# Performance work log

Measured on AMD Instinct MI355X. Metric: run time of the kernel, lower is better.

## Reference

```python
import jax, jax.numpy as jnp
import numpy as np

B, S, E, H = 8, 1024, 1024, 16
D = E // H  # per-head dim = 64
STD = 0.05  # nn.init.normal_ std used in the torch module


def setup_inputs() -> dict:
    key = jax.random.key(0)
    ks = jax.random.split(key, 9)
    inputs = jax.random.normal(ks[0], (B, S, E), dtype=jnp.float32)
    mlp_params_Q = jax.random.normal(ks[1], (B, E), dtype=jnp.float32)
    mlp_params_K = jax.random.normal(ks[2], (B, E), dtype=jnp.float32)
    W_Query = jax.random.normal(ks[3], (E, E), dtype=jnp.float32) * STD
    W_Key = jax.random.normal(ks[4], (E, E), dtype=jnp.float32) * STD
    W_Value = jax.random.normal(ks[5], (E, E), dtype=jnp.float32) * STD
    W_Out = jax.random.normal(ks[6], (E, E), dtype=jnp.float32) * STD  # nn.Linear weight [out, in]
    ln_gamma = jax.random.normal(ks[7], (E,), dtype=jnp.float32) * STD
    ln_beta = jax.random.normal(ks[8], (E,), dtype=jnp.float32) * STD
    return {"inputs": inputs, "mlp_params_Q": mlp_params_Q, "mlp_params_K": mlp_params_K,
            "W_Query": W_Query, "W_Key": W_Key, "W_Value": W_Value, "W_Out": W_Out,
            "ln_gamma": ln_gamma, "ln_beta": ln_beta}


def reference(inputs, mlp_params_Q, mlp_params_K, W_Query, W_Key, W_Value, W_Out, ln_gamma, ln_beta):
    # QKV projections: [B,S,E] @ [E,E]
    q = jnp.einsum('bse,ef->bsf', inputs, W_Query)
    k = jnp.einsum('bse,ef->bsf', inputs, W_Key)
    v = jnp.einsum('bse,ef->bsf', inputs, W_Value)
    # meta gate modulation (flag='gate', mode='QK'): per-batch channel gates, *2
    q = q * mlp_params_Q[:, None, :] * 2.0
    k = k * mlp_params_K[:, None, :] * 2.0
    # split heads: channels [h*D:(h+1)*D] -> head h (matches torch.split/stack)
    qh = q.reshape(B, S, H, D)
    kh = k.reshape(B, S, H, D)
    vh = v.reshape(B, S, H, D)
    # attention scores [B,H,S,S], scaled by sqrt(D)
    scores = jnp.einsum('bihd,bjhd->bhij', qh, kh) / jnp.sqrt(jnp.asarray(D, q.dtype))
    attn = jax.nn.softmax(scores, axis=-1)  # attn_dropout is identity at eval
    out = jnp.einsum('bhij,bjhd->bihd', attn, vh).reshape(B, S, E)  # concat heads
    # output projection (nn.Linear, no bias): x @ W.T; dropout identity at eval
    res = jnp.einsum('bse,fe->bsf', out, W_Out)
    # residual + LayerNorm(eps=1e-6)
    res = res + inputs
    mean = jnp.mean(res, axis=-1, keepdims=True)
    var = jnp.mean(jnp.square(res - mean), axis=-1, keepdims=True)
    res = (res - mean) * jax.lax.rsqrt(var + 1e-6) * ln_gamma + ln_beta
    return res
```

## Files before the change

### kernel.cpp

```cpp
#include <hip/hip_runtime.h>
#include <stdint.h>

#define Bn 8
#define Sn 1024
#define En 1024
#define Hn 16
#define Dn 64
#define Mn (Bn*Sn)

typedef unsigned short u16;
typedef _Float16 f16;
typedef _Float16 f16x8 __attribute__((ext_vector_type(8)));
typedef __fp16   h16x2 __attribute__((ext_vector_type(2)));
typedef float    f32x4 __attribute__((ext_vector_type(4)));

static __device__ __forceinline__ u16 f2h(float x){
  f16 h = (f16)x;
  union { f16 h; u16 u; } c; c.h = h; return c.u;
}
static __device__ __forceinline__ f32x4 mfma16(f16x8 a, f16x8 b, f32x4 c){
  return __builtin_amdgcn_mfma_f32_16x16x32_f16(a, b, c, 0, 0, 0);
}
static __device__ __forceinline__ void gl_lds16(const u16* g, u16* l){
  __builtin_amdgcn_global_load_lds((__attribute__((address_space(1))) void*)g,
                                   (__attribute__((address_space(3))) void*)l, 16, 0, 0);
}

__global__ __launch_bounds__(256) void k_cvt_x(const float* __restrict__ x,
                                               u16* __restrict__ o){
  int i = blockIdx.x*256 + threadIdx.x;
  float4 v = ((const float4*)x)[i];
  ushort4 h; h.x = f2h(v.x); h.y = f2h(v.y); h.z = f2h(v.z); h.w = f2h(v.w);
  ((ushort4*)o)[i] = h;
}

__global__ __launch_bounds__(256) void k_prep_w(const float* __restrict__ Wq,
    const float* __restrict__ Wk, const float* __restrict__ Wv,
    u16* __restrict__ wq, u16* __restrict__ wk, u16* __restrict__ wv){
  __shared__ float t[32][33];
  int tx = threadIdx.x & 31, ty = threadIdx.x >> 5;
  int bx = blockIdx.x & 31, by = blockIdx.x >> 5;
  const float* W = (blockIdx.y == 0) ? Wq : (blockIdx.y == 1) ? Wk : Wv;
  u16* D = (blockIdx.y == 0) ? wq : (blockIdx.y == 1) ? wk : wv;
  for (int i = 0; i < 32; i += 8)
    t[ty+i][tx] = W[(size_t)(by*32+ty+i)*En + bx*32+tx];
  __syncthreads();
  for (int i = 0; i < 32; i += 8)
    D[(size_t)(bx*32+ty+i)*En + by*32+tx] = f2h(t[tx][ty+i]);
}

__global__ __launch_bounds__(256) void k_conv(const float* __restrict__ w,
                                              u16* __restrict__ o){
  int i = blockIdx.x*256 + threadIdx.x;
  float4 v = ((const float4*)w)[i];
  ushort4 h; h.x = f2h(v.x); h.y = f2h(v.y); h.z = f2h(v.z); h.w = f2h(v.w);
  ((ushort4*)o)[i] = h;
}

__global__ __launch_bounds__(256) void k_gemm_g(
    const u16* __restrict__ A, const u16* __restrict__ Bw,
    const float* __restrict__ gate, float gscale, u16* __restrict__ C){
  __shared__ u16 sA[128*32], sB[128*32];
  const int t = threadIdx.x, w = t >> 6, l = t & 63;
  const int lr = l & 15, lg = l >> 4;
  const int tn = blockIdx.x & 7, tm = blockIdx.x >> 3;
  const int m0 = tm*128, n0 = tn*128;
  const int wr = (w >> 1)*64, wc = (w & 1)*64;
  f32x4 acc[4][4] = {};
  for (int k0 = 0; k0 < En; k0 += 32){
    for (int c = 0; c < 2; c++){
      int ch  = c*256 + t;
      int row = ch >> 2;
      int xb  = (ch & 3) << 4;
      int col = k0 + ((xb ^ ((row & 3) << 4)) >> 1);
      int ldso = (c*256 + w*64) * 16;
      gl_lds16(A  + (size_t)(m0+row)*En + col, (u16*)((char*)sA + ldso));
      gl_lds16(Bw + (size_t)(n0+row)*En + col, (u16*)((char*)sB + ldso));
    }
    __syncthreads();
    f16x8 af[4], bf[4];
    #pragma unroll
    for (int i = 0; i < 4; i++){
      int r  = wr + i*16 + lr;
      af[i] = *(const f16x8*)((const char*)sA + r*64 + ((lg*16) ^ ((r & 3) << 4)));
      int n  = wc + i*16 + lr;
      bf[i] = *(const f16x8*)((const char*)sB + n*64 + ((lg*16) ^ ((n & 3) << 4)));
    }
    #pragma unroll
    for (int i = 0; i < 4; i++)
      #pragma unroll
      for (int j = 0; j < 4; j++)
        acc[i][j] = mfma16(af[i], bf[j], acc[i][j]);
    __syncthreads();
  }
  const int bb = m0 >> 10;
  #pragma unroll
  for (int j = 0; j < 4; j++){
    int col = n0 + wc + j*16 + lr;
    float g = gate[bb*En + col] * gscale;
    #pragma unroll
    for (int i = 0; i < 4; i++){
      int mbase = m0 + wr + i*16 + lg*4;
      #pragma unroll
      for (int r = 0; r < 4; r++)
        C[(size_t)(mbase + r)*En + col] = f2h(acc[i][j][r] * g);
    }
  }
}

template<int MODE>
__global__ __launch_bounds__(256) void k_gemm1(
    const u16* __restrict__ A, const u16* __restrict__ Bw,
    const float* __restrict__ resid, u16* __restrict__ Cb, float* __restrict__ Cf){
  __shared__ u16 sA[128*32], sB[128*32];
  const int t = threadIdx.x, w = t >> 6, l = t & 63;
  const int lr = l & 15, lg = l >> 4;
  const int tn = blockIdx.x & 7, tm = blockIdx.x >> 3;
  const int m0 = tm*128, n0 = tn*128;
  const int wr = (w >> 1)*64, wc = (w & 1)*64;
  f32x4 acc[4][4] = {};
  for (int k0 = 0; k0 < En; k0 += 32){
    for (int c = 0; c < 2; c++){
      int ch  = c*256 + t;
      int row = ch >> 2;
      int xb  = (ch & 3) << 4;
      int col = k0 + ((xb ^ ((row & 3) << 4)) >> 1);
      int ldso = (c*256 + w*64) * 16;
      gl_lds16(A  + (size_t)(m0+row)*En + col, (u16*)((char*)sA + ldso));
      gl_lds16(Bw + (size_t)(n0+row)*En + col, (u16*)((char*)sB + ldso));
    }
    __syncthreads();
    f16x8 af[4], bf[4];
    #pragma unroll
    for (int i = 0; i < 4; i++){
      int r  = wr + i*16 + lr;
      af[i] = *(const f16x8*)((const char*)sA + r*64 + ((lg*16) ^ ((r & 3) << 4)));
      int n  = wc + i*16 + lr;
      bf[i] = *(const f16x8*)((const char*)sB + n*64 + ((lg*16) ^ ((n & 3) << 4)));
    }
    #pragma unroll
    for (int i = 0; i < 4; i++)
      #pragma unroll
      for (int j = 0; j < 4; j++)
        acc[i][j] = mfma16(af[i], bf[j], acc[i][j]);
    __syncthreads();
  }
  if (MODE == 0){
    const int bb = m0 >> 10, s0 = (m0 & 1023) + wr;
    #pragma unroll
    for (int j = 0; j < 4; j++){
      int n = n0 + wc + j*16 + lr;
      int hh = n >> 6, d = n & 63;
      u16* dst = Cb + ((size_t)(bb*Hn + hh)*Dn + d)*Sn;
      #pragma unroll
      for (int i = 0; i < 4; i++){
        int ss = s0 + i*16 + lg*4;
        ushort4 pk;
        pk.x = f2h(acc[i][j][0]); pk.y = f2h(acc[i][j][1]);
        pk.z = f2h(acc[i][j][2]); pk.w = f2h(acc[i][j][3]);
        *(ushort4*)&dst[ss] = pk;
      }
    }
  } else {
    #pragma unroll
    for (int j = 0; j < 4; j++){
      int col = n0 + wc + j*16 + lr;
      #pragma unroll
      for (int i = 0; i < 4; i++){
        int mbase = m0 + wr + i*16 + lg*4;
        #pragma unroll
        for (int r = 0; r < 4; r++){
          size_t o = (size_t)(mbase + r)*En + col;
          Cf[o] = acc[i][j][r] + resid[o];
        }
      }
    }
  }
}

__global__ __launch_bounds__(256) void k_attn(
    const u16* __restrict__ qp, const u16* __restrict__ kp,
    const u16* __restrict__ vt, u16* __restrict__ outp){
  __shared__ u16 sK[64*64];
  __shared__ u16 sVt[64*64];
  __shared__ u16 sP[4][16*72];
  const int t = threadIdx.x, w = t >> 6, l = t & 63;
  const int lr = l & 15, lg = l >> 4;
  const int qt = blockIdx.x & 15, h = (blockIdx.x >> 4) & 15, b = blockIdx.x >> 8;
  const int q0 = qt*64 + w*16;

  size_t qrow = (size_t)(b*Sn + q0 + lr)*En + h*Dn;
  f16x8 qf[2];
  #pragma unroll
  for (int ks = 0; ks < 2; ks++)
    qf[ks] = *(const f16x8*)&qp[qrow + ks*32 + lg*8];
  f32x4 accO[4] = {};
  float mrun = -1e30f, lrun = 0.f;
  u16* P = &sP[w][0];

  for (int kt = 0; kt < Sn/64; kt++){
    for (int c = 0; c < 2; c++){
      int ch = c*256 + t, row = ch >> 3, slot = ch & 7;
      int jc = slot ^ (row & 7);
      int ldso = (c*256 + w*64) * 16;
      size_t gk = (size_t)(b*Sn + kt*64 + row)*En + h*Dn + jc*8;
      gl_lds16(kp + gk, (u16*)((char*)sK + ldso));
      size_t gv = ((size_t)(b*Hn + h)*Dn + row)*Sn + kt*64 + jc*8;
      gl_lds16(vt + gv, (u16*)((char*)sVt + ldso));
    }
    __syncthreads();
    f32x4 s[4] = {};
    __builtin_amdgcn_s_setprio(1);
    #pragma unroll
    for (int ks = 0; ks < 2; ks++)
      #pragma unroll
      for (int jt = 0; jt < 4; jt++){
        int j  = jt*16 + lr;
        int ob = j*128 + ((ks*64 + lg*16) ^ ((j & 7) << 4));
        f16x8 kf = *(const f16x8*)((const char*)sK + ob);
        s[jt] = mfma16(kf, qf[ks], s[jt]);
      }
    __builtin_amdgcn_s_setprio(0);
    float m16 = fmaxf(fmaxf(fmaxf(s[0][0], s[0][1]), fmaxf(s[0][2], s[0][3])),
                      fmaxf(fmaxf(s[1][0], s[1][1]), fmaxf(s[1][2], s[1][3])));
    m16 = fmaxf(m16, fmaxf(fmaxf(fmaxf(s[2][0], s[2][1]), fmaxf(s[2][2], s[2][3])),
                           fmaxf(fmaxf(s[3][0], s[3][1]), fmaxf(s[3][2], s[3][3]))));
    m16 = fmaxf(m16, __shfl_xor(m16, 16));
    m16 = fmaxf(m16, __shfl_xor(m16, 32));
    bool defer = __all(m16 <= mrun + 8.0f);
    float mn, sc;
    if (defer){ mn = mrun; sc = 1.0f; }
    else { mn = fmaxf(mrun, m16); sc = exp2f(mrun - mn); mrun = mn; }
    float ps = 0.f;
    #pragma unroll
    for (int jt = 0; jt < 4; jt++){
      float p0 = exp2f(s[jt][0] - mn), p1 = exp2f(s[jt][1] - mn);
      float p2 = exp2f(s[jt][2] - mn), p3 = exp2f(s[jt][3] - mn);
      ps += (p0 + p1) + (p2 + p3);
      union { h16x2 h; uint32_t u; } ca, cb;
      ca.h = __builtin_amdgcn_cvt_pkrtz(p0, p1);
      cb.h = __builtin_amdgcn_cvt_pkrtz(p2, p3);
      uint2 pk; pk.x = ca.u; pk.y = cb.u;
      *(uint2*)&P[lr*72 + jt*16 + lg*4] = pk;
    }
    ps += __shfl_xor(ps, 16);
    ps += __shfl_xor(ps, 32);
    lrun = lrun*sc + ps;
    if (!defer){
      #pragma unroll
      for (int r = 0; r < 4; r++){
        float scq = __shfl(sc, lg*4 + r);
        accO[0][r] *= scq; accO[1][r] *= scq;
        accO[2][r] *= scq; accO[3][r] *= scq;
      }
    }
    __builtin_amdgcn_s_setprio(1);
    #pragma unroll
    for (int js = 0; js < 2; js++){
      f16x8 pa = *(const f16x8*)&P[lr*72 + js*32 + lg*8];
      #pragma unroll
      for (int dt = 0; dt < 4; dt++){
        int d  = dt*16 + lr;
        int ob = d*128 + ((lg*16 + js*64) ^ ((d & 7) << 4));
        f16x8 vb = *(const f16x8*)((const char*)sVt + ob);
        accO[dt] = mfma16(pa, vb, accO[dt]);
      }
    }
    __builtin_amdgcn_s_setprio(0);
    __syncthreads();
  }
  float inv = 1.0f / lrun;
  float ir[4];
  #pragma unroll
  for (int r = 0; r < 4; r++) ir[r] = __shfl(inv, lg*4 + r);
  #pragma unroll
  for (int dt = 0; dt < 4; dt++){
    int dcol = h*Dn + dt*16 + lr;
    #pragma unroll
    for (int r = 0; r < 4; r++)
      outp[(size_t)(b*Sn + q0 + lg*4 + r)*En + dcol] = f2h(accO[dt][r] * ir[r]);
  }
}

__global__ __launch_bounds__(256) void k_ln(const float* __restrict__ res,
    const float* __restrict__ gamma, const float* __restrict__ beta,
    float* __restrict__ out){
  int row = blockIdx.x, t = threadIdx.x;
  const float* r = res + (size_t)row*En;
  float4 v = ((const float4*)r)[t];
  float s = v.x + v.y + v.z + v.w;
  float q = v.x*v.x + v.y*v.y + v.z*v.z + v.w*v.w;
  for (int d = 1; d < 64; d <<= 1){ s += __shfl_xor(s, d); q += __shfl_xor(q, d); }
  __shared__ float ss[4], sq[4];
  int w = t >> 6, l = t & 63;
  if (l == 0){ ss[w] = s; sq[w] = q; }
  __syncthreads();
  s = ss[0] + ss[1] + ss[2] + ss[3];
  q = sq[0] + sq[1] + sq[2] + sq[3];
  float mean = s * (1.f/En);
  float var  = q * (1.f/En) - mean*mean;
  float rs   = rsqrtf(var + 1e-6f);
  float4 g = ((const float4*)gamma)[t], bb = ((const float4*)beta)[t];
  float4 o;
  o.x = (v.x - mean)*rs*g.x + bb.x;
  o.y = (v.y - mean)*rs*g.y + bb.y;
  o.z = (v.z - mean)*rs*g.z + bb.z;
  o.w = (v.w - mean)*rs*g.w + bb.w;
  ((float4*)(out + (size_t)row*En))[t] = o;
}

extern "C" void kernel_launch(void* const* d_in, const int* in_sizes, int n_in,
                              void* d_out, int out_size, void* d_ws, size_t ws_size,
                              hipStream_t stream){
  (void)in_sizes; (void)n_in; (void)out_size; (void)ws_size;
  const float* X     = (const float*)d_in[0];
  const float* gQ    = (const float*)d_in[1];
  const float* gK    = (const float*)d_in[2];
  const float* Wq    = (const float*)d_in[3];
  const float* Wk    = (const float*)d_in[4];
  const float* Wv    = (const float*)d_in[5];
  const float* Wo    = (const float*)d_in[6];
  const float* gamma = (const float*)d_in[7];
  const float* beta  = (const float*)d_in[8];
  float* out = (float*)d_out;

  char* ws = (char*)d_ws;
  const size_t sz = (size_t)Mn*En*2;
  u16* xh = (u16*)(ws + 0*sz);
  u16* qh = (u16*)(ws + 1*sz);
  u16* kh = (u16*)(ws + 2*sz);
  u16* vb = (u16*)(ws + 3*sz);
  u16* ao = (u16*)(ws + 4*sz);
  float* res = (float*)(ws + 0*sz);
  u16* wq = (u16*)(ws + 5*sz);
  u16* wk = wq + (size_t)En*En;
  u16* wv = wk + (size_t)En*En;
  u16* wo = wv + (size_t)En*En;

  k_cvt_x<<<Mn*En/1024, 256, 0, stream>>>(X, xh);
  k_prep_w<<<dim3((En/32)*(En/32), 3), 256, 0, stream>>>(Wq, Wk, Wv, wq, wk, wv);
  k_conv<<<En*En/1024, 256, 0, stream>>>(Wo, wo);
  k_gemm_g<<<(Mn/128)*(En/128), 256, 0, stream>>>(xh, wq, gQ, 0.25f*1.4426950408889634f, qh);
  k_gemm_g<<<(Mn/128)*(En/128), 256, 0, stream>>>(xh, wk, gK, 2.0f, kh);
  k_gemm1<0><<<(Mn/128)*(En/128), 256, 0, stream>>>(xh, wv, nullptr, vb, nullptr);
  k_attn<<<Bn*Hn*(Sn/64), 256, 0, stream>>>(qh, kh, vb, ao);
  k_gemm1<1><<<(Mn/128)*(En/128), 256, 0, stream>>>(ao, wo, X, nullptr, res);
  k_ln<<<Mn, 256, 0, stream>>>(res, gamma, beta, out);
}
```

Measured before the change: 320.4 us.

## Fuse QKV GEMMs into one launch and double-buffer attention K/V tiles

The three Q/K/V projection GEMMs become one launch over a 3E-wide output, relying on wq/wk/wv sitting contiguously in the workspace, with the epilogue choosing the gate and output by column block. The attention kernel moves to 512-thread blocks of 128 queries and double-buffers K/V tiles in LDS, using vmcnt waits and raw barriers so the next tile's load overlaps the current tile's compute. MFMA priority hints are also added to the GEMMs. The aim is fewer launches, better K/V reuse and hidden load latency, at the cost of twice the attention LDS and reliance on hand-placed waitcnt ordering.

```diff
diff --git a/kernel.cpp b/kernel.cpp
--- a/kernel.cpp
+++ b/kernel.cpp
@@ -13,6 +13,9 @@
 typedef _Float16 f16x8 __attribute__((ext_vector_type(8)));
 typedef __fp16   h16x2 __attribute__((ext_vector_type(2)));
 typedef float    f32x4 __attribute__((ext_vector_type(4)));
+
+#define VMCNT(n) asm volatile("s_waitcnt vmcnt(" #n ")" ::: "memory")
+#define CFENCE() asm volatile("" ::: "memory")
 
 static __device__ __forceinline__ u16 f2h(float x){
   f16 h = (f16)x;
@@ -57,9 +60,85 @@
   ((ushort4*)o)[i] = h;
 }
 
-__global__ __launch_bounds__(256) void k_gemm_g(
+__global__ __launch_bounds__(256) void k_gemm_qkv(
     const u16* __restrict__ A, const u16* __restrict__ Bw,
-    const float* __restrict__ gate, float gscale, u16* __restrict__ C){
+    const float* __restrict__ gQ, const float* __restrict__ gK,
+    u16* __restrict__ Cq, u16* __restrict__ Ck, u16* __restrict__ Vt){
+  __shared__ u16 sA[128*32], sB[128*32];
+  const int t = threadIdx.x, w = t >> 6, l = t & 63;
+  const int lr = l & 15, lg = l >> 4;
+  const int tn = blockIdx.x % 24, tm = blockIdx.x / 24;
+  const int m0 = tm*128, n0 = tn*128;
+  const int wr = (w >> 1)*64, wc = (w & 1)*64;
+  f32x4 acc[4][4] = {};
+  for (int k0 = 0; k0 < En; k0 += 32){
+    for (int c = 0; c < 2; c++){
+      int ch  = c*256 + t;
+      int row = ch >> 2;
+      int xb  = (ch & 3) << 4;
+      int col = k0 + ((xb ^ ((row & 3) << 4)) >> 1);
+      int ldso = (c*256 + w*64) * 16;
+      gl_lds16(A  + (size_t)(m0+row)*En + col, (u16*)((char*)sA + ldso));
+      gl_lds16(Bw + (size_t)(n0+row)*En + col, (u16*)((char*)sB + ldso));
+    }
+    __syncthreads();
+    f16x8 af[4], bf[4];
+    #pragma unroll
+    for (int i = 0; i < 4; i++){
+      int r  = wr + i*16 + lr;
+      af[i] = *(const f16x8*)((const char*)sA + r*64 + ((lg*16) ^ ((r & 3) << 4)));
+      int n  = wc + i*16 + lr;
+      bf[i] = *(const f16x8*)((const char*)sB + n*64 + ((lg*16) ^ ((n & 3) << 4)));
+    }
+    __builtin_amdgcn_s_setprio(1);
+    #pragma unroll
+    for (int i = 0; i < 4; i++)
+      #pragma unroll
+      for (int j = 0; j < 4; j++)
+        acc[i][j] = mfma16(af[i], bf[j], acc[i][j]);
+    __builtin_amdgcn_s_setprio(0);
+    __syncthreads();
+  }
+  const int bb = m0 >> 10;
+  const int sel = n0 >> 10;
+  if (sel < 2){
+    const float* gate = sel ? gK : gQ;
+    const float gs = sel ? 2.0f : 0.25f*1.4426950408889634f;
+    u16* C = sel ? Ck : Cq;
+    #pragma unroll
+    for (int j = 0; j < 4; j++){
+      int col = (n0 & 1023) + wc + j*16 + lr;
+      float g = gate[bb*En + col] * gs;
+      #pragma unroll
+      for (int i = 0; i < 4; i++){
+        int mbase = m0 + wr + i*16 + lg*4;
+        #pragma unroll
+        for (int r = 0; r < 4; r++)
+          C[(size_t)(mbase + r)*En + col] = f2h(acc[i][j][r] * g);
+      }
+    }
+  } else {
+    const int s0 = (m0 & 1023) + wr;
+    #pragma unroll
+    for (int j = 0; j < 4; j++){
+      int nn = (n0 - 2048) + wc + j*16 + lr;
+      int hh = nn >> 6, d = nn & 63;
+      u16* dst = Vt + ((size_t)(bb*Hn + hh)*Dn + d)*Sn;
+      #pragma unroll
+      for (int i = 0; i < 4; i++){
+        int ss = s0 + i*16 + lg*4;
+        ushort4 pk;
+        pk.x = f2h(acc[i][j][0]); pk.y = f2h(acc[i][j][1]);
+        pk.z = f2h(acc[i][j][2]); pk.w = f2h(acc[i][j][3]);
+        *(ushort4*)&dst[ss] = pk;
+      }
+    }
+  }
+}
+
+__global__ __launch_bounds__(256) void k_gemm_out(
+    const u16* __restrict__ A, const u16* __restrict__ Bw,
+    const float* __restrict__ resid, float* __restrict__ Cf){
   __shared__ u16 sA[128*32], sB[128*32];
   const int t = threadIdx.x, w = t >> 6, l = t & 63;
   const int lr = l & 15, lg = l >> 4;
@@ -86,108 +165,50 @@
       int n  = wc + i*16 + lr;
       bf[i] = *(const f16x8*)((const char*)sB + n*64 + ((lg*16) ^ ((n & 3) << 4)));
     }
+    __builtin_amdgcn_s_setprio(1);
     #pragma unroll
     for (int i = 0; i < 4; i++)
       #pragma unroll
       for (int j = 0; j < 4; j++)
         acc[i][j] = mfma16(af[i], bf[j], acc[i][j]);
+    __builtin_amdgcn_s_setprio(0);
     __syncthreads();
   }
-  const int bb = m0 >> 10;
   #pragma unroll
   for (int j = 0; j < 4; j++){
     int col = n0 + wc + j*16 + lr;
-    float g = gate[bb*En + col] * gscale;
     #pragma unroll
     for (int i = 0; i < 4; i++){
       int mbase = m0 + wr + i*16 + lg*4;
       #pragma unroll
-      for (int r = 0; r < 4; r++)
-        C[(size_t)(mbase + r)*En + col] = f2h(acc[i][j][r] * g);
-    }
-  }
-}
-
-template<int MODE>
-__global__ __launch_bounds__(256) void k_gemm1(
-    const u16* __restrict__ A, const u16* __restrict__ Bw,
-    const float* __restrict__ resid, u16* __restrict__ Cb, float* __restrict__ Cf){
-  __shared__ u16 sA[128*32], sB[128*32];
+      for (int r = 0; r < 4; r++){
+        size_t o = (size_t)(mbase + r)*En + col;
+        Cf[o] = acc[i][j][r] + resid[o];
+      }
+    }
+  }
+}
+
+__global__ __launch_bounds__(512) void k_attn(
+    const u16* __restrict__ qp, const u16* __restrict__ kp,
+    const u16* __restrict__ vt, u16* __restrict__ outp){
+  __shared__ u16 sK[2][64*64];
+  __shared__ u16 sVt[2][64*64];
+  __shared__ u16 sP[8][16*72];
   const int t = threadIdx.x, w = t >> 6, l = t & 63;
   const int lr = l & 15, lg = l >> 4;
-  const int tn = blockIdx.x & 7, tm = blockIdx.x >> 3;
-  const int m0 = tm*128, n0 = tn*128;
-  const int wr = (w >> 1)*64, wc = (w & 1)*64;
-  f32x4 acc[4][4] = {};
-  for (int k0 = 0; k0 < En; k0 += 32){
-    for (int c = 0; c < 2; c++){
-      int ch  = c*256 + t;
-      int row = ch >> 2;
-      int xb  = (ch & 3) << 4;
-      int col = k0 + ((xb ^ ((row & 3) << 4)) >> 1);
-      int ldso = (c*256 + w*64) * 16;
-      gl_lds16(A  + (size_t)(m0+row)*En + col, (u16*)((char*)sA + ldso));
-      gl_lds16(Bw + (size_t)(n0+row)*En + col, (u16*)((char*)sB + ldso));
-    }
-    __syncthreads();
-    f16x8 af[4], bf[4];
-    #pragma unroll
-    for (int i = 0; i < 4; i++){
-      int r  = wr + i*16 + lr;
-      af[i] = *(const f16x8*)((const char*)sA + r*64 + ((lg*16) ^ ((r & 3) << 4)));
-      int n  = wc + i*16 + lr;
-      bf[i] = *(const f16x8*)((const char*)sB + n*64 + ((lg*16) ^ ((n & 3) << 4)));
-    }
-    #pragma unroll
-    for (int i = 0; i < 4; i++)
-      #pragma unroll
-      for (int j = 0; j < 4; j++)
-        acc[i][j] = mfma16(af[i], bf[j], acc[i][j]);
-    __syncthreads();
-  }
-  if (MODE == 0){
-    const int bb = m0 >> 10, s0 = (m0 & 1023) + wr;
-    #pragma unroll
-    for (int j = 0; j < 4; j++){
-      int n = n0 + wc + j*16 + lr;
-      int hh = n >> 6, d = n & 63;
-      u16* dst = Cb + ((size_t)(bb*Hn + hh)*Dn + d)*Sn;
-      #pragma unroll
-      for (int i = 0; i < 4; i++){
-        int ss = s0 + i*16 + lg*4;
-        ushort4 pk;
-        pk.x = f2h(acc[i][j][0]); pk.y = f2h(acc[i][j][1]);
-        pk.z = f2h(acc[i][j][2]); pk.w = f2h(acc[i][j][3]);
-        *(ushort4*)&dst[ss] = pk;
-      }
-    }
-  } else {
-    #pragma unroll
-    for (int j = 0; j < 4; j++){
-      int col = n0 + wc + j*16 + lr;
-      #pragma unroll
-      for (int i = 0; i < 4; i++){
-        int mbase = m0 + wr + i*16 + lg*4;
-        #pragma unroll
-        for (int r = 0; r < 4; r++){
-          size_t o = (size_t)(mbase + r)*En + col;
-          Cf[o] = acc[i][j][r] + resid[o];
-        }
-      }
-    }
-  }
-}
-
-__global__ __launch_bounds__(256) void k_attn(
-    const u16* __restrict__ qp, const u16* __restrict__ kp,
-    const u16* __restrict__ vt, u16* __restrict__ outp){
-  __shared__ u16 sK[64*64];
-  __shared__ u16 sVt[64*64];
-  __shared__ u16 sP[4][16*72];
-  const int t = threadIdx.x, w = t >> 6, l = t & 63;
-  const int lr = l & 15, lg = l >> 4;
-  const int qt = blockIdx.x & 15, h = (blockIdx.x >> 4) & 15, b = blockIdx.x >> 8;
-  const int q0 = qt*64 + w*16;
+  const int qt = blockIdx.x >> 7, hb = blockIdx.x & 127;
+  const int h = hb & 15, b = hb >> 4;
+  const int q0 = qt*128 + w*16;
+
+  const int srow = t >> 3, slot = t & 7, jc = slot ^ (srow & 7);
+  const size_t gkbase = (size_t)(b*Sn + srow)*En + h*Dn + jc*8;
+  const size_t gvbase = ((size_t)(b*Hn + h)*Dn + srow)*Sn + jc*8;
+
+#define STAGE(buf, kt_) do { \
+    gl_lds16(kp + gkbase + (size_t)(kt_)*64*En, (u16*)((char*)sK[buf] + w*1024)); \
+    gl_lds16(vt + gvbase + (kt_)*64,            (u16*)((char*)sVt[buf] + w*1024)); \
+  } while (0)
 
   size_t qrow = (size_t)(b*Sn + q0 + lr)*En + h*Dn;
   f16x8 qf[2];
@@ -198,17 +219,13 @@
   float mrun = -1e30f, lrun = 0.f;
   u16* P = &sP[w][0];
 
+  STAGE(0, 0);
   for (int kt = 0; kt < Sn/64; kt++){
-    for (int c = 0; c < 2; c++){
-      int ch = c*256 + t, row = ch >> 3, slot = ch & 7;
-      int jc = slot ^ (row & 7);
-      int ldso = (c*256 + w*64) * 16;
-      size_t gk = (size_t)(b*Sn + kt*64 + row)*En + h*Dn + jc*8;
-      gl_lds16(kp + gk, (u16*)((char*)sK + ldso));
-      size_t gv = ((size_t)(b*Hn + h)*Dn + row)*Sn + kt*64 + jc*8;
-      gl_lds16(vt + gv, (u16*)((char*)sVt + ldso));
-    }
-    __syncthreads();
+    const int cur = kt & 1;
+    if (kt < Sn/64 - 1){ STAGE(cur^1, kt+1); VMCNT(2); }
+    else               { VMCNT(0); }
+    __builtin_amdgcn_s_barrier();
+    CFENCE();
     f32x4 s[4] = {};
     __builtin_amdgcn_s_setprio(1);
     #pragma unroll
@@ -217,7 +234,7 @@
       for (int jt = 0; jt < 4; jt++){
         int j  = jt*16 + lr;
         int ob = j*128 + ((ks*64 + lg*16) ^ ((j & 7) << 4));
-        f16x8 kf = *(const f16x8*)((const char*)sK + ob);
+        f16x8 kf = *(const f16x8*)((const char*)sK[cur] + ob);
         s[jt] = mfma16(kf, qf[ks], s[jt]);
       }
     __builtin_amdgcn_s_setprio(0);
@@ -262,13 +279,17 @@
       for (int dt = 0; dt < 4; dt++){
         int d  = dt*16 + lr;
         int ob = d*128 + ((lg*16 + js*64) ^ ((d & 7) << 4));
-        f16x8 vb = *(const f16x8*)((const char*)sVt + ob);
+        f16x8 vb = *(const f16x8*)((const char*)sVt[cur] + ob);
         accO[dt] = mfma16(pa, vb, accO[dt]);
       }
     }
     __builtin_amdgcn_s_setprio(0);
-    __syncthreads();
-  }
+    if (kt < Sn/64 - 1){
+      CFENCE();
+      __builtin_amdgcn_s_barrier();
+    }
+  }
+#undef STAGE
   float inv = 1.0f / lrun;
   float ir[4];
   #pragma unroll
@@ -340,10 +361,8 @@
   k_cvt_x<<<Mn*En/1024, 256, 0, stream>>>(X, xh);
   k_prep_w<<<dim3((En/32)*(En/32), 3), 256, 0, stream>>>(Wq, Wk, Wv, wq, wk, wv);
   k_conv<<<En*En/1024, 256, 0, stream>>>(Wo, wo);
-  k_gemm_g<<<(Mn/128)*(En/128), 256, 0, stream>>>(xh, wq, gQ, 0.25f*1.4426950408889634f, qh);
-  k_gemm_g<<<(Mn/128)*(En/128), 256, 0, stream>>>(xh, wk, gK, 2.0f, kh);
-  k_gemm1<0><<<(Mn/128)*(En/128), 256, 0, stream>>>(xh, wv, nullptr, vb, nullptr);
-  k_attn<<<Bn*Hn*(Sn/64), 256, 0, stream>>>(qh, kh, vb, ao);
-  k_gemm1<1><<<(Mn/128)*(En/128), 256, 0, stream>>>(ao, wo, X, nullptr, res);
+  k_gemm_qkv<<<(Mn/128)*(3*En/128), 256, 0, stream>>>(xh, wq, gQ, gK, qh, kh, vb);
+  k_attn<<<(Sn/128)*Hn*Bn, 512, 0, stream>>>(qh, kh, vb, ao);
+  k_gemm_out<<<(Mn/128)*(En/128), 256, 0, stream>>>(ao, wo, X, res);
   k_ln<<<Mn, 256, 0, stream>>>(res, gamma, beta, out);
 }
```

Result: faster. 297.0 us (-7.3%).
